# Performance work log

Measured on AMD Instinct MI355X. Metric: run time of the kernel, lower is better.

## Reference

```python
import jax, jax.numpy as jnp
import numpy as np

K = 20
EPS = 1e-5
NUM_CLASSES = 50


def knn_idx(x, k):
    # x: [B, C, N] -> [B, N, k] indices of k nearest neighbors (self included)
    xx = jnp.sum(x * x, axis=1)                      # [B, N]
    inner = jnp.einsum('bcn,bcm->bnm', x, x)         # [B, N, N]
    neg_dist = 2.0 * inner - xx[:, :, None] - xx[:, None, :]
    return jax.lax.top_k(neg_dist, k)[1]


def graph_feature(x, k):
    # x: [B, C, N] -> [B, 2C, N, k] edge features (feat - center, center)
    B = x.shape[0]
    idx = knn_idx(x, k)                              # [B, N, k]
    xt = jnp.transpose(x, (0, 2, 1))                 # [B, N, C]
    feat = xt[jnp.arange(B)[:, None, None], idx]     # [B, N, k, C]
    center = xt[:, :, None, :]
    out = jnp.concatenate([feat - center, jnp.broadcast_to(center, feat.shape)], axis=-1)
    return jnp.transpose(out, (0, 3, 1, 2))


def group_norm(x, groups, w, b):
    B, C = x.shape[0], x.shape[1]
    shp = x.shape
    xg = x.reshape(B, groups, -1)
    mu = jnp.mean(xg, axis=-1, keepdims=True)
    var = jnp.var(xg, axis=-1, keepdims=True)
    xn = ((xg - mu) * jax.lax.rsqrt(var + EPS)).reshape(shp)
    bshape = (1, C) + (1,) * (len(shp) - 2)
    return xn * w.reshape(bshape) + b.reshape(bshape)


def leaky(x):
    return jnp.where(x >= 0, x, 0.2 * x)


def edge_block(x, W, gw, gb, groups, k):
    f = graph_feature(x, k)                          # [B, 2C, N, k]
    h = jnp.einsum('oc,bcnk->bonk', W, f)            # 1x1 conv2d, no bias
    h = leaky(group_norm(h, groups, gw, gb))
    return jnp.max(h, axis=-1)                       # [B, Cout, N]


def conv1d(x, W, b):
    return jnp.einsum('oc,bcn->bon', W, x) + b[None, :, None]


def _mk(key, shape, fan_in):
    return jax.random.normal(key, shape, jnp.float32) * (1.0 / np.sqrt(fan_in))


def setup_inputs():
    key = jax.random.key(0)
    ks = jax.random.split(key, 32)
    B, N = 8, 2048
    d = {}
    d['x'] = jax.random.normal(ks[0], (B, 3, N), jnp.float32)
    d['W1'] = _mk(ks[1], (64, 6), 6)
    d['W2'] = _mk(ks[2], (64, 128), 128)
    d['W3'] = _mk(ks[3], (128, 128), 128)
    for i, (name, c) in enumerate([('g1', 64), ('g2', 64), ('g3', 128), ('gf', 1024), ('gs1', 512), ('gs2', 256), ('gs3', 128)]):
        d[name + 'w'] = 1.0 + 0.02 * jax.random.normal(ks[4 + 2 * i], (c,), jnp.float32)
        d[name + 'b'] = 0.02 * jax.random.normal(ks[5 + 2 * i], (c,), jnp.float32)
    d['Wm'] = _mk(ks[20], (1024, 256), 256)
    d['bm'] = jnp.zeros((1024,), jnp.float32)
    d['Ws1'] = _mk(ks[21], (512, 1280), 1280)
    d['bs1'] = jnp.zeros((512,), jnp.float32)
    d['Ws2'] = _mk(ks[22], (256, 512), 512)
    d['bs2'] = jnp.zeros((256,), jnp.float32)
    d['Ws3'] = _mk(ks[23], (128, 256), 256)
    d['bs3'] = jnp.zeros((128,), jnp.float32)
    d['Ws4'] = _mk(ks[24], (NUM_CLASSES, 128), 128)
    d['bs4'] = jnp.zeros((NUM_CLASSES,), jnp.float32)
    return d


def reference(x, W1, W2, W3, g1w, g1b, g2w, g2b, g3w, g3b, gfw, gfb, gs1w, gs1b, gs2w, gs2b, gs3w, gs3b, Wm, bm, Ws1, bs1, Ws2, bs2, Ws3, bs3, Ws4, bs4):
    B, _, N = x.shape
    x1 = edge_block(x, W1, g1w, g1b, 8, K)           # [B, 64, N]
    x2 = edge_block(x1, W2, g2w, g2b, 8, K)          # [B, 64, N]
    x3 = edge_block(x2, W3, g3w, g3b, 8, K)          # [B, 128, N]
    feats = jnp.concatenate([x1, x2, x3], axis=1)    # [B, 256, N]
    xb = jax.nn.relu(group_norm(conv1d(feats, Wm, bm), 32, gfw, gfb))  # [B, 1024, N]
    xmax = jnp.max(xb, axis=2)                       # [B, 1024]
    xmax_exp = jnp.broadcast_to(xmax[:, :, None], (B, 1024, N))
    combined = jnp.concatenate([xmax_exp, feats], axis=1)  # [B, 1280, N]
    h = jax.nn.relu(group_norm(conv1d(combined, Ws1, bs1), 16, gs1w, gs1b))
    h = jax.nn.relu(group_norm(conv1d(h, Ws2, bs2), 16, gs2w, gs2b))
    h = jax.nn.relu(group_norm(conv1d(h, Ws3, bs3), 8, gs3w, gs3b))
    logits = conv1d(h, Ws4, bs4)                     # [B, num_classes, N]
    return jax.nn.log_softmax(logits, axis=1)
```

## Files before the change

### kernel.cpp

```cpp
#include <hip/hip_runtime.h>

#define BN 8
#define NP 2048
#define KK 20
#define EPSV 1e-5f

typedef __attribute__((ext_vector_type(8))) short bf16x8;
typedef __attribute__((ext_vector_type(4))) float f32x4;

static __device__ __forceinline__ float leakyf(float v){ return v >= 0.f ? v : 0.2f*v; }
static __device__ __forceinline__ unsigned fenc(float f){
  unsigned u = __float_as_uint(f);
  unsigned m = (unsigned)((int)u >> 31);
  return u ^ (m | 0x80000000u);
}
static __device__ __forceinline__ float fdec(unsigned u){
  return __uint_as_float((u & 0x80000000u) ? (u & 0x7FFFFFFFu) : ~u);
}
static __device__ __forceinline__ unsigned bf2(float a, float b){
  unsigned ua = __float_as_uint(a), ub = __float_as_uint(b);
  ua = (ua + 0x7FFFu + ((ua>>16)&1u)) >> 16;
  ub = (ub + 0x7FFFu + ((ub>>16)&1u)) >> 16;
  return ua | (ub<<16);
}
static __device__ __forceinline__ unsigned short b16(float v){
  unsigned u = __float_as_uint(v);
  return (unsigned short)((u + 0x7FFFu + ((u>>16)&1u)) >> 16);
}
static __device__ __forceinline__ unsigned umax32(unsigned a, unsigned b){ return __builtin_elementwise_max(a,b); }
static __device__ __forceinline__ unsigned med3u(unsigned a, unsigned b, unsigned c){
  unsigned d;
  asm("v_med3_u32 %0, %1, %2, %3" : "=v"(d) : "v"(a), "v"(b), "v"(c));
  return d;
}

static __device__ __forceinline__ char* ldsW(char* base, int row, int colb){
  return base + row*80 + (colb ^ ((((unsigned)row>>3)&3u)<<4));
}
static __device__ __forceinline__ char* ldsX(char* base, int row, int colb){
  return base + row*80 + (colb ^ (((((unsigned)row>>2)^((unsigned)row>>4))&3u)<<4));
}
static __device__ __forceinline__ int swz128(int row, int colb){
  return (colb ^ ((row&7)<<4));
}

__global__ __launch_bounds__(256) void xx_kernel(const float* __restrict__ x, long ldb, int C,
                                                 float* __restrict__ xx){
  int b = blockIdx.y;
  int n = blockIdx.x*256 + threadIdx.x;
  const float* xp = x + (long)b*ldb + n;
  float a = 0.f;
  for(int c=0;c<C;c++){ float v = xp[(long)c*NP]; a += v*v; }
  xx[b*NP + n] = a;
}

static __device__ __forceinline__ void ins20(unsigned* tv, unsigned key){
  unsigned pold = tv[0];
  tv[0] = umax32(tv[0], key);
  #pragma unroll
  for(int r=1;r<20;r++){
    unsigned cold = tv[r];
    tv[r] = med3u(key, pold, cold);
    pold = cold;
  }
}

__global__ __launch_bounds__(256) void knnf_kernel(const unsigned short* __restrict__ fh,
                                                   const unsigned short* __restrict__ fl,
                                                   int cbase,
                                                   const float* __restrict__ xx,
                                                   unsigned* __restrict__ pk){
  __shared__ unsigned short CH[64][68];
  __shared__ unsigned short CL[64][68];
  __shared__ unsigned SK[64][68];
  __shared__ float cxs[64];
  const int b    = blockIdx.z;
  const int part = blockIdx.y;
  const int q0   = blockIdx.x*64;
  const int t    = threadIdx.x;
  const int lane = t & 63;
  const int w    = t >> 6;
  const int lr   = lane & 15, lg = lane >> 4;
  const unsigned short* fhb = fh + (long)b*NP*256;
  const unsigned short* flb = fl + (long)b*NP*128;
  const float* xxb = xx + b*NP;

  const unsigned short* qa = fhb + ((long)(q0 + w*16 + lr))*256 + cbase + lg*8;
  const unsigned short* qb = flb + ((long)(q0 + w*16 + lr))*128 + cbase + lg*8;
  bf16x8 ah0 = *(const bf16x8*)(qa);
  bf16x8 ah1 = *(const bf16x8*)(qa + 32);
  bf16x8 al0 = *(const bf16x8*)(qb);
  bf16x8 al1 = *(const bf16x8*)(qb + 32);
  float4 qxx4 = *(const float4*)(xxb + q0 + w*16 + lg*4);
  float qxx[4] = {qxx4.x, qxx4.y, qxx4.z, qxx4.w};

  unsigned tv[20];
  #pragma unroll
  for(int r=0;r<20;r++) tv[r] = 0u;
  const int sq = t>>2, sl = t&3;

  #define STAGE(ct_)                                                                        \
    {                                                                                       \
      const int ct__ = (ct_);                                                               \
      _Pragma("unroll")                                                                     \
      for(int i = t; i < 512; i += 256){                                                    \
        int row = i >> 3, seg = i & 7;                                                      \
        *(uint4*)&CH[row][seg*8] = *(const uint4*)(fhb + ((long)(ct__*64+row))*256 + cbase + seg*8); \
        *(uint4*)&CL[row][seg*8] = *(const uint4*)(flb + ((long)(ct__*64+row))*128 + cbase + seg*8); \
      }                                                                                     \
      if (t < 64) cxs[t] = xxb[ct__*64 + t];                                                \
    }

  STAGE(part*4);
  __syncthreads();

  #pragma unroll
  for(int cc=0; cc<4; cc++){
    __builtin_amdgcn_s_setprio(1);
    f32x4 acc[4];
    #pragma unroll
    for(int nt=0; nt<4; nt++){
      int crow = nt*16 + lr;
      bf16x8 bh0 = *(const bf16x8*)&CH[crow][lg*8];
      bf16x8 bh1 = *(const bf16x8*)&CH[crow][32 + lg*8];
      bf16x8 bl0 = *(const bf16x8*)&CL[crow][lg*8];
      bf16x8 bl1 = *(const bf16x8*)&CL[crow][32 + lg*8];
      f32x4 a = (f32x4){0.f,0.f,0.f,0.f};
      a = __builtin_amdgcn_mfma_f32_16x16x32_bf16(ah0, bh0, a, 0,0,0);
      a = __builtin_amdgcn_mfma_f32_16x16x32_bf16(ah1, bh1, a, 0,0,0);
      a = __builtin_amdgcn_mfma_f32_16x16x32_bf16(ah0, bl0, a, 0,0,0);
      a = __builtin_amdgcn_mfma_f32_16x16x32_bf16(ah1, bl1, a, 0,0,0);
      a = __builtin_amdgcn_mfma_f32_16x16x32_bf16(al0, bh0, a, 0,0,0);
      a = __builtin_amdgcn_mfma_f32_16x16x32_bf16(al1, bh1, a, 0,0,0);
      acc[nt] = a;
    }
    __builtin_amdgcn_s_setprio(0);
    float cxv[4];
    #pragma unroll
    for(int nt=0; nt<4; nt++) cxv[nt] = cxs[nt*16 + lr];
    unsigned key4[4][4];
    #pragma unroll
    for(int nt=0; nt<4; nt++){
      #pragma unroll
      for(int r=0;r<4;r++){
        float neg = 2.f*acc[nt][r] - qxx[r] - cxv[nt];
        key4[nt][r] = (fenc(neg) & 0xFFFFFF00u) | (255u - (unsigned)(cc*64 + nt*16 + lr));
      }
    }
    __syncthreads();
    #pragma unroll
    for(int nt=0; nt<4; nt++)
      #pragma unroll
      for(int r=0;r<4;r++)
        SK[w*16 + lg*4 + r][nt*16 + lr] = key4[nt][r];
    if (cc < 3){
      STAGE(part*4 + cc + 1);
    }
    __syncthreads();
    #pragma unroll
    for(int jj=0;jj<4;jj++){
      uint4 kv = *(const uint4*)&SK[sq][sl*16 + jj*4];
      ins20(tv, kv.x); ins20(tv, kv.y); ins20(tv, kv.z); ins20(tv, kv.w);
    }
  }
  #undef STAGE
  long base = ((((long)b*NP + q0 + sq)*8 + part)*4 + sl)*20;
  #pragma unroll
  for(int r=0;r<20;r++) pk[base+r] = tv[r];
}

__global__ __launch_bounds__(256) void knn1_kernel(const float* __restrict__ x,
                                                   const float* __restrict__ xx,
                                                   unsigned* __restrict__ pk){
  __shared__ float cx0[256], cx1[256], cx2[256], cxxa[256];
  const int b    = blockIdx.z;
  const int part = blockIdx.y;
  const int q0   = blockIdx.x*64;
  const int t    = threadIdx.x;
  const float* xb  = x + (long)b*3*NP;
  const float* xxb = xx + b*NP;

  cx0[t]  = xb[part*256 + t];
  cx1[t]  = xb[NP + part*256 + t];
  cx2[t]  = xb[2*NP + part*256 + t];
  cxxa[t] = xxb[part*256 + t];

  const int sq = t>>2, sl = t&3;
  const int q = q0 + sq;
  float qx = xb[q], qy = xb[NP + q], qz = xb[2*NP + q];
  float qxx = xxb[q];
  __syncthreads();

  unsigned tv[20];
  #pragma unroll
  for(int r=0;r<20;r++) tv[r] = 0u;

  for(int cc=0; cc<4; cc++){
    #pragma unroll
    for(int j=0;j<16;j++){
      int m = cc*64 + sl*16 + j;
      float ip = qx*cx0[m] + qy*cx1[m] + qz*cx2[m];
      float neg = 2.f*ip - qxx - cxxa[m];
      unsigned key = (fenc(neg) & 0xFFFFFF00u) | (255u - (unsigned)m);
      ins20(tv, key);
    }
  }
  long base = ((((long)b*NP + q0 + sq)*8 + part)*4 + sl)*20;
  #pragma unroll
  for(int r=0;r<20;r++) pk[base+r] = tv[r];
}

__global__ __launch_bounds__(256) void knnmerge_kernel(const unsigned* __restrict__ pk,
                                                       int* __restrict__ idxout){
  const int wid  = threadIdx.x >> 6;
  const int lane = threadIdx.x & 63;
  const long qg = (long)blockIdx.x*4 + wid;
  const unsigned* kb = pk + qg*640;
  const int l = lane >> 1, h = lane & 1;
  unsigned k[10];
  {
    const unsigned* src = kb + l*20 + h*10;
    #pragma unroll
    for(int i=0;i<10;i++) k[i] = src[i];
  }
  int rem = 10;
  int* op = idxout + qg*KK;
  const int gbase = (l>>2)*256;
  for(int r=0;r<KK;r++){
    unsigned key = k[0];
    int gi = gbase + 255 - (int)(key & 255u);
    unsigned long long cmp = (rem > 0)
        ? ((unsigned long long)(key & 0xFFFFFF00u) << 32) | (unsigned)(0x7FFFFFFF - gi)
        : 0ull;
    unsigned long long w = cmp;
    #pragma unroll
    for(int s=1;s<64;s<<=1){
      unsigned long long o = __shfl_xor(w, s, 64);
      w = (o > w) ? o : w;
    }
    if (lane == 0){
      op[r] = 0x7FFFFFFF - (int)(unsigned)(w & 0xFFFFFFFFu);
    }
    if (cmp == w){
      #pragma unroll
      for(int i=0;i<9;i++) k[i] = k[i+1];
      rem--;
    }
  }
}

template<int CIN, int O>
__global__ __launch_bounds__(256) void pcdual_kernel(const float* __restrict__ x, long ldb,
                                                     const float* __restrict__ W,
                                                     float* __restrict__ ya, float* __restrict__ dd){
  __shared__ float Wt[CIN][O+1];
  constexpr int NLOC = 256/O;
  const int b = blockIdx.y;
  const int n0 = blockIdx.x*NLOC;
  const int t = threadIdx.x;
  const int o = t % O;
  const int n = n0 + t/O;
  const float* xp = x + (long)b*ldb + n;
  float xv[CIN];
  #pragma unroll
  for(int c=0;c<CIN;c++) xv[c] = xp[(long)c*NP];
  for(int i=t;i<CIN*O;i+=256){ int oo=i/CIN, c=i%CIN; Wt[c][oo] = W[(long)oo*2*CIN + c]; }
  __syncthreads();
  float aa = 0.f;
  #pragma unroll
  for(int c=0;c<CIN;c++) aa += Wt[c][o]*xv[c];
  __syncthreads();
  for(int i=t;i<CIN*O;i+=256){ int oo=i/CIN, c=i%CIN; Wt[c][oo] = W[(long)oo*2*CIN + CIN + c]; }
  __syncthreads();
  float ab = 0.f;
  #pragma unroll
  for(int c=0;c<CIN;c++) ab += Wt[c][o]*xv[c];
  long outoff = ((long)b*NP + n)*O + o;
  ya[outoff] = aa;
  dd[outoff] = ab - aa;
}

template<int O>
__global__ __launch_bounds__(256) void pcdualm_kernel(const unsigned short* __restrict__ fh,
                                                      const unsigned short* __restrict__ fl,
                                                      int cbase,
                                                      const float* __restrict__ W,
                                                      float* __restrict__ ya, float* __restrict__ dd){
  __shared__ unsigned short AH[O][64];
  __shared__ unsigned short AL[O][64];
  __shared__ unsigned short DH[O][64];
  __shared__ unsigned short DL[O][64];
  const int b  = blockIdx.y;
  const int n0 = blockIdx.x*64;
  const int t  = threadIdx.x;
  const int lane = t & 63;
  const int w  = t >> 6;
  const int lr = lane & 15, lg = lane >> 4;

  for(int i=t; i<O*64; i+=256){
    int o = i >> 6, c = i & 63;
    float va = W[(long)o*128 + c];
    float vb = W[(long)o*128 + 64 + c];
    float vd = vb - va;
    unsigned short ah = b16(va);
    unsigned short dh = b16(vd);
    int byt = swz128(o, c*2);
    *(unsigned short*)((char*)&AH[o][0] + byt) = ah;
    *(unsigned short*)((char*)&AL[o][0] + byt) = b16(va - __uint_as_float(((unsigned)ah)<<16));
    *(unsigned short*)((char*)&DH[o][0] + byt) = dh;
    *(unsigned short*)((char*)&DL[o][0] + byt) = b16(vd - __uint_as_float(((unsigned)dh)<<16));
  }

  const int n = n0 + w*16 + lr;
  const unsigned short* xh = fh + ((long)b*NP + n)*256 + cbase + lg*8;
  const unsigned short* xl = fl + ((long)b*NP + n)*128 + cbase + lg*8;
  bf16x8 xh0 = *(const bf16x8*)(xh);
  bf16x8 xh1 = *(const bf16x8*)(xh + 32);
  bf16x8 xl0 = *(const bf16x8*)(xl);
  bf16x8 xl1 = *(const bf16x8*)(xl + 32);
  __syncthreads();

  #pragma unroll
  for(int mi=0; mi<O/16; mi++){
    int row = mi*16 + lr;
    bf16x8 a_h0 = *(const bf16x8*)((char*)&AH[row][0] + swz128(row, lg*16));
    bf16x8 a_h1 = *(const bf16x8*)((char*)&AH[row][0] + swz128(row, 64 + lg*16));
    bf16x8 a_l0 = *(const bf16x8*)((char*)&AL[row][0] + swz128(row, lg*16));
    bf16x8 a_l1 = *(const bf16x8*)((char*)&AL[row][0] + swz128(row, 64 + lg*16));
    f32x4 aa = (f32x4){0.f,0.f,0.f,0.f};
    aa = __builtin_amdgcn_mfma_f32_16x16x32_bf16(a_h0, xh0, aa, 0,0,0);
    aa = __builtin_amdgcn_mfma_f32_16x16x32_bf16(a_h1, xh1, aa, 0,0,0);
    aa = __builtin_amdgcn_mfma_f32_16x16x32_bf16(a_h0, xl0, aa, 0,0,0);
    aa = __builtin_amdgcn_mfma_f32_16x16x32_bf16(a_h1, xl1, aa, 0,0,0);
    aa = __builtin_amdgcn_mfma_f32_16x16x32_bf16(a_l0, xh0, aa, 0,0,0);
    aa = __builtin_amdgcn_mfma_f32_16x16x32_bf16(a_l1, xh1, aa, 0,0,0);
    bf16x8 d_h0 = *(const bf16x8*)((char*)&DH[row][0] + swz128(row, lg*16));
    bf16x8 d_h1 = *(const bf16x8*)((char*)&DH[row][0] + swz128(row, 64 + lg*16));
    bf16x8 d_l0 = *(const bf16x8*)((char*)&DL[row][0] + swz128(row, lg*16));
    bf16x8 d_l1 = *(const bf16x8*)((char*)&DL[row][0] + swz128(row, 64 + lg*16));
    f32x4 ad = (f32x4){0.f,0.f,0.f,0.f};
    ad = __builtin_amdgcn_mfma_f32_16x16x32_bf16(d_h0, xh0, ad, 0,0,0);
    ad = __builtin_amdgcn_mfma_f32_16x16x32_bf16(d_h1, xh1, ad, 0,0,0);
    ad = __builtin_amdgcn_mfma_f32_16x16x32_bf16(d_h0, xl0, ad, 0,0,0);
    ad = __builtin_amdgcn_mfma_f32_16x16x32_bf16(d_h1, xl1, ad, 0,0,0);
    ad = __builtin_amdgcn_mfma_f32_16x16x32_bf16(d_l0, xh0, ad, 0,0,0);
    ad = __builtin_amdgcn_mfma_f32_16x16x32_bf16(d_l1, xh1, ad, 0,0,0);
    long ooff = ((long)b*NP + n)*O + mi*16 + lg*4;
    float4 va = {aa[0],aa[1],aa[2],aa[3]};
    float4 vd = {ad[0],ad[1],ad[2],ad[3]};
    *(float4*)(ya + ooff) = va;
    *(float4*)(dd + ooff) = vd;
  }
}

template<int O>
__global__ __launch_bounds__(256) void egather_kernel(const float* __restrict__ ya, const float* __restrict__ dd,
                               const int* __restrict__ idx,
                               float* __restrict__ mx, float* __restrict__ mn,
                               float* __restrict__ stats){
  __shared__ float sred2[4][16];
  constexpr int NSUB = 256/O;
  constexpr int CPG = O/8;
  const int b  = blockIdx.x & 7;
  const int n0 = (blockIdx.x >> 3) * 32;
  const int t = threadIdx.x;
  const int w = t >> 6;
  const int o = t % O;
  const int ns = t / O;
  if (t < 64) sred2[t>>4][t&15] = 0.f;
  __syncthreads();
  float gs = 0.f, gs2 = 0.f;
  const float* yab = ya + (long)b*NP*O;
  for(int p=ns; p<32; p+=NSUB){
    int n = n0 + p;
    float d = dd[((long)b*NP + n)*O + o];
    const int* ip = idx + ((long)b*NP + n)*KK;
    float m = -__builtin_inff(), mm = __builtin_inff(), s = 0.f, s2 = 0.f;
    #pragma unroll
    for(int k=0;k<KK;k++){
      int j = ip[k];
      float v = yab[(long)j*O + o] + d;
      s += v; s2 += v*v;
      m = fmaxf(m, v); mm = fminf(mm, v);
    }
    mx[((long)b*NP + n)*O + o] = m;
    mn[((long)b*NP + n)*O + o] = mm;
    gs += s; gs2 += s2;
  }
  #pragma unroll
  for(int offm=1; offm<CPG; offm<<=1){
    gs  += __shfl_xor(gs,  offm, CPG);
    gs2 += __shfl_xor(gs2, offm, CPG);
  }
  if ((o & (CPG-1)) == 0){
    int g = o / CPG;
    sred2[w][g*2]   = gs;
    sred2[w][g*2+1] = gs2;
  }
  __syncthreads();
  if (t < 16){
    float a = sred2[0][t] + sred2[1][t] + sred2[2][t] + sred2[3][t];
    atomicAdd(&stats[b*16 + t], a);
  }
}

template<int O, bool NEEDXX, bool WRITEL>
__global__ __launch_bounds__(256) void enorm_kernel(const float* __restrict__ mx, const float* __restrict__ mn,
                                                    const float* __restrict__ stats,
                                                    const float* __restrict__ gw, const float* __restrict__ gb,
                                                    int coff,
                                                    float* __restrict__ xxout,
                                                    unsigned* __restrict__ fhout, unsigned* __restrict__ flout){
  __shared__ float lmx[64][65];
  __shared__ float lmn[64][65];
  const int b = blockIdx.z;
  const int o0 = blockIdx.y*64;
  const int n0 = blockIdx.x*64;
  const int t = threadIdx.x;
  for(int r=0;r<16;r++){
    int i = r*4 + t/64, j = t%64;
    long src = ((long)b*NP + n0 + i)*O + o0 + j;
    lmx[i][j] = mx[src];
    lmn[i][j] = mn[src];
  }
  __syncthreads();
  constexpr int CPG = O/8;
  const float inv_cnt = 1.f/((float)CPG*NP*KK);
  float xacc = 0.f;
  for(int r=0;r<16;r++){
    int ol = r*4 + t/64, nl = t%64;
    int og = o0 + ol;
    int g = og / CPG;
    float S  = stats[(b*8+g)*2];
    float S2 = stats[(b*8+g)*2+1];
    float mu = S*inv_cnt;
    float var = S2*inv_cnt - mu*mu;
    float rs = rsqrtf(var + EPSV);
    float w = gw[og], bb = gb[og];
    float sel = (w >= 0.f) ? lmx[nl][ol] : lmn[nl][ol];
    float v = leakyf((sel - mu)*rs*w + bb);
    lmx[nl][ol] = v;
    if (NEEDXX) xacc += v*v;
  }
  __syncthreads();
  {
    const int cb2 = (coff + o0) >> 1;
    #pragma unroll
    for(int k=0;k<8;k++){
      int flat = k*256 + t;
      int n = flat >> 5, cp = flat & 31;
      float v0 = lmx[n][2*cp], v1 = lmx[n][2*cp+1];
      unsigned short h0 = b16(v0), h1 = b16(v1);
      fhout[((long)b*NP + n0 + n)*128 + cb2 + cp] = (unsigned)h0 | ((unsigned)h1<<16);
      if (WRITEL){
        float r0 = v0 - __uint_as_float(((unsigned)h0)<<16);
        float r1 = v1 - __uint_as_float(((unsigned)h1)<<16);
        flout[((long)b*NP + n0 + n)*64 + cb2 + cp] =
            (unsigned)b16(r0) | ((unsigned)b16(r1)<<16);
      }
    }
  }
  if (NEEDXX){
    __syncthreads();
    float* red = &lmn[0][0];
    red[(t>>6)*64 + (t&63)] = xacc;
    __syncthreads();
    if (t < 64){
      float a = red[t] + red[64+t] + red[128+t] + red[192+t];
      xxout[b*NP + n0 + t] = a;
    }
  }
}

template<bool WRITE_Y, bool DO_STATS, bool DO_MAXMIN, bool IN_NORM, bool XBF16>
__global__ __launch_bounds__(256) void mgemm_kernel(
    const float* __restrict__ W, int ldw,
    const float* __restrict__ x, long xldb,
    const unsigned short* __restrict__ xbf,
    const float* __restrict__ bias, const float* __restrict__ basev,
    int O, int C, int gshift,
    float* __restrict__ y, float* __restrict__ stats,
    unsigned* __restrict__ mmax, unsigned* __restrict__ mmin,
    const float* __restrict__ instats, const float* __restrict__ igw,
    const float* __restrict__ igb, int igshift, float iinv)
{
  __shared__ __align__(16) char WlB[128*80];
  __shared__ __align__(16) char XtB[XBF16 ? 16 : 128*80];
  __shared__ float sred[16];
  __shared__ unsigned smax[128];
  __shared__ unsigned smin[128];

  const int b  = blockIdx.z;
  const int o0 = blockIdx.y*128;
  const int nb = blockIdx.x*128;
  const int t  = threadIdx.x;
  const int lane = t & 63;
  const int wid = t >> 6;
  const int wmo = wid >> 1, wno = wid & 1;
  const int lr = lane & 15, lg = lane >> 4;

  if (DO_STATS && t < 16) sred[t] = 0.f;
  if (DO_MAXMIN && t < 128){ smax[t] = 0u; smin[t] = 0xFFFFFFFFu; }

  f32x4 acc[4][4];
  #pragma unroll
  for(int i=0;i<4;i++)
    #pragma unroll
    for(int j=0;j<4;j++) acc[i][j] = (f32x4){0.f,0.f,0.f,0.f};

  const int so  = t & 127;
  const int scb = (t >> 7) << 5;
  const int xcg = t >> 5;
  const int xng = t & 31;

  for(int cc=0; cc<C; cc+=32){
    bf16x8 bfr[4];
    if (XBF16){
      #pragma unroll
      for(int nj=0;nj<4;nj++)
        bfr[nj] = *(const bf16x8*)(xbf + ((long)b*NP + nb + wno*64 + nj*16 + lr)*256 + cc + lg*8);
    }
    __syncthreads();
    {
      const float* wp = W + (long)(o0 + so)*ldw + cc + (scb>>1);
      #pragma unroll
      for(int j=0;j<4;j++){
        float4 f = *(const float4*)(wp + j*4);
        uint2 v = { bf2(f.x,f.y), bf2(f.z,f.w) };
        *(uint2*)ldsW(WlB, so, scb + j*8) = v;
      }
    }
    if (!XBF16){
      const float* xp = x + (long)b*xldb + (long)(cc + xcg*4)*NP + nb + xng*4;
      float4 f0 = *(const float4*)(xp);
      float4 f1 = *(const float4*)(xp + NP);
      float4 f2 = *(const float4*)(xp + 2*NP);
      float4 f3 = *(const float4*)(xp + 3*NP);
      float X4[4][4] = {{f0.x,f0.y,f0.z,f0.w},{f1.x,f1.y,f1.z,f1.w},
                        {f2.x,f2.y,f2.z,f2.w},{f3.x,f3.y,f3.z,f3.w}};
      if (IN_NORM){
        #pragma unroll
        for(int i=0;i<4;i++){
          int c = cc + xcg*4 + i;
          int g = c >> igshift;
          const float* sp = instats + ((long)b*(C>>igshift) + g)*2;
          float mu = sp[0]*iinv;
          float var = sp[1]*iinv - mu*mu;
          float rs = rsqrtf(var + EPSV);
          float aa = rs*igw[c];
          float c2 = igb[c] - mu*aa;
          #pragma unroll
          for(int j=0;j<4;j++) X4[i][j] = fmaxf(X4[i][j]*aa + c2, 0.f);
        }
      }
      #pragma unroll
      for(int j=0;j<4;j++){
        uint2 v = { bf2(X4[0][j], X4[1][j]), bf2(X4[2][j], X4[3][j]) };
        *(uint2*)ldsX(XtB, xng*4 + j, xcg*8) = v;
      }
    }
    __syncthreads();
    bf16x8 afr[4];
    #pragma unroll
    for(int mi=0;mi<4;mi++) afr[mi] = *(const bf16x8*)ldsW(WlB, wmo*64 + mi*16 + lr, lg*16);
    if (!XBF16){
      #pragma unroll
      for(int nj=0;nj<4;nj++) bfr[nj] = *(const bf16x8*)ldsX(XtB, wno*64 + nj*16 + lr, lg*16);
    }
    #pragma unroll
    for(int mi=0;mi<4;mi++)
      #pragma unroll
      for(int nj=0;nj<4;nj++)
        acc[mi][nj] = __builtin_amdgcn_mfma_f32_16x16x32_bf16(afr[mi], bfr[nj], acc[mi][nj], 0, 0, 0);
  }

  float bb4[4][4];
  #pragma unroll
  for(int mi=0;mi<4;mi++){
    #pragma unroll
    for(int r=0;r<4;r++){
      int o = o0 + wmo*64 + mi*16 + lg*4 + r;
      float v = 0.f;
      if (bias)  v += bias[o];
      if (basev) v += basev[(long)b*O + o];
      bb4[mi][r] = v;
    }
  }
  #pragma unroll
  for(int mi=0;mi<4;mi++)
    #pragma unroll
    for(int nj=0;nj<4;nj++)
      #pragma unroll
      for(int r=0;r<4;r++) acc[mi][nj][r] += bb4[mi][r];

  if (WRITE_Y){
    #pragma unroll
    for(int mi=0;mi<4;mi++)
      #pragma unroll
      for(int nj=0;nj<4;nj++)
        #pragma unroll
        for(int r=0;r<4;r++){
          int o = o0 + wmo*64 + mi*16 + lg*4 + r;
          y[((long)b*O + o)*NP + nb + wno*64 + nj*16 + lr] = acc[mi][nj][r];
        }
  }
  if (DO_STATS){
    #pragma unroll
    for(int mi=0;mi<4;mi++){
      float s = 0.f, s2 = 0.f;
      #pragma unroll
      for(int nj=0;nj<4;nj++)
        #pragma unroll
        for(int r=0;r<4;r++){ float v = acc[mi][nj][r]; s += v; s2 += v*v; }
      int gi = (wmo*64 + mi*16) >> gshift;
      atomicAdd(&sred[gi*2],   s);
      atomicAdd(&sred[gi*2+1], s2);
    }
  }
  if (DO_MAXMIN){
    #pragma unroll
    for(int mi=0;mi<4;mi++)
      #pragma unroll
      for(int r=0;r<4;r++){
        float mv = acc[mi][0][r], mw = acc[mi][0][r];
        #pragma unroll
        for(int nj=1;nj<4;nj++){ mv = fmaxf(mv, acc[mi][nj][r]); mw = fminf(mw, acc[mi][nj][r]); }
        int ol = wmo*64 + mi*16 + lg*4 + r;
        atomicMax(&smax[ol], fenc(mv));
        atomicMin(&smin[ol], fenc(mw));
      }
  }
  if (DO_STATS || DO_MAXMIN) __syncthreads();
  if (DO_STATS){
    int ngb = 128 >> gshift;
    if (t < ngb*2){
      atomicAdd(&stats[((long)b*(O>>gshift) + (o0>>gshift) + (t>>1))*2 + (t&1)], sred[t]);
    }
  }
  if (DO_MAXMIN){
    if (t < 128){
      atomicMax(&mmax[(long)b*O + o0 + t], smax[t]);
      atomicMin(&mmin[(long)b*O + o0 + t], smin[t]);
    }
  }
}

__global__ void xmax_kernel(const unsigned* __restrict__ mmax, const unsigned* __restrict__ mmin,
                            const float* __restrict__ stats, const float* __restrict__ gw,
                            const float* __restrict__ gb, float* __restrict__ xmax){
  int t = blockIdx.x*256 + threadIdx.x;
  int b = t >> 10, o = t & 1023;
  int g = o >> 5;
  const float* sp = stats + (b*32+g)*2;
  const float inv_cnt = 1.f/(32.f*NP);
  float mu = sp[0]*inv_cnt;
  float var = sp[1]*inv_cnt - mu*mu;
  float rs = rsqrtf(var + EPSV);
  float w = gw[o];
  float sel = (w >= 0.f) ? fdec(mmax[t]) : fdec(mmin[t]);
  float v = (sel - mu)*rs*w + gb[o];
  xmax[t] = fmaxf(v, 0.f);
}

__global__ __launch_bounds__(256) void base1_kernel(const float* __restrict__ Ws1, const float* __restrict__ bs1,
                                                    const float* __restrict__ xmax, float* __restrict__ base1){
  __shared__ float sred[4][8];
  const int o = blockIdx.x;
  const int t = threadIdx.x;
  const float* wp = Ws1 + (long)o*1280;
  float acc[8];
  #pragma unroll
  for(int bb=0;bb<8;bb++) acc[bb]=0.f;
  #pragma unroll
  for(int cc=0;cc<4;cc++){
    int c = cc*256 + t;
    float w = wp[c];
    #pragma unroll
    for(int bb=0;bb<8;bb++) acc[bb] += w * xmax[bb*1024 + c];
  }
  #pragma unroll
  for(int bb=0;bb<8;bb++){
    float a = acc[bb];
    a += __shfl_xor(a,1);  a += __shfl_xor(a,2);  a += __shfl_xor(a,4);
    a += __shfl_xor(a,8);  a += __shfl_xor(a,16); a += __shfl_xor(a,32);
    acc[bb]=a;
  }
  if ((t&63)==0){
    #pragma unroll
    for(int bb=0;bb<8;bb++) sred[t>>6][bb]=acc[bb];
  }
  __syncthreads();
  if (t<8){
    float a = sred[0][t]+sred[1][t]+sred[2][t]+sred[3][t] + bs1[o];
    base1[t*512 + o] = a;
  }
}

__global__ __launch_bounds__(256) void s4_kernel(const float* __restrict__ h3raw,
                                                 const float* __restrict__ stats,
                                                 const float* __restrict__ gw, const float* __restrict__ gb,
                                                 const float* __restrict__ W,
                                                 const float* __restrict__ bias,
                                                 float* __restrict__ out){
  const int b = blockIdx.y;
  const int n = blockIdx.x*64 + (threadIdx.x>>2);
  const int cl = threadIdx.x & 3;
  const float inv_cnt = 1.f/(16.f*NP);
  float mu0, rs0, mu1, rs1;
  {
    const float* sp = stats + (b*8 + cl*2)*2;
    mu0 = sp[0]*inv_cnt;
    float var = sp[1]*inv_cnt - mu0*mu0;
    rs0 = rsqrtf(var + EPSV);
    const float* sp1 = stats + (b*8 + cl*2 + 1)*2;
    mu1 = sp1[0]*inv_cnt;
    float var1 = sp1[1]*inv_cnt - mu1*mu1;
    rs1 = rsqrtf(var1 + EPSV);
  }
  float hv[32];
  #pragma unroll
  for(int c=0;c<32;c++){
    int og = cl*32 + c;
    float rs = (c < 16) ? rs0 : rs1;
    float mu = (c < 16) ? mu0 : mu1;
    float a = rs*gw[og];
    float c2 = gb[og] - mu*a;
    float v = h3raw[((long)b*128 + og)*NP + n];
    hv[c] = fmaxf(v*a + c2, 0.f);
  }
  float zz[50];
  #pragma unroll
  for(int o=0;o<50;o++){
    const float* wp = W + o*128 + cl*32;
    float a = 0.f;
    #pragma unroll
    for(int c=0;c<32;c++) a += wp[c]*hv[c];
    a += __shfl_xor(a,1);
    a += __shfl_xor(a,2);
    zz[o] = a + bias[o];
  }
  float m = zz[0];
  #pragma unroll
  for(int o=1;o<50;o++) m = fmaxf(m, zz[o]);
  float s = 0.f;
  #pragma unroll
  for(int o=0;o<50;o++) s += __expf(zz[o]-m);
  float lse = m + __logf(s);
  #pragma unroll
  for(int o=0;o<50;o++){
    if ((o&3)==cl) out[((long)b*50+o)*NP+n] = zz[o]-lse;
  }
}

extern "C" void kernel_launch(void* const* d_in, const int* in_sizes, int n_in,
                              void* d_out, int out_size, void* d_ws, size_t ws_size,
                              hipStream_t stream)
{
  const float* x   = (const float*)d_in[0];
  const float* W1  = (const float*)d_in[1];
  const float* W2  = (const float*)d_in[2];
  const float* W3  = (const float*)d_in[3];
  const float* g1w = (const float*)d_in[4];
  const float* g1b = (const float*)d_in[5];
  const float* g2w = (const float*)d_in[6];
  const float* g2b = (const float*)d_in[7];
  const float* g3w = (const float*)d_in[8];
  const float* g3b = (const float*)d_in[9];
  const float* gfw = (const float*)d_in[10];
  const float* gfb = (const float*)d_in[11];
  const float* gs1w= (const float*)d_in[12];
  const float* gs1b= (const float*)d_in[13];
  const float* gs2w= (const float*)d_in[14];
  const float* gs2b= (const float*)d_in[15];
  const float* gs3w= (const float*)d_in[16];
  const float* gs3b= (const float*)d_in[17];
  const float* Wm  = (const float*)d_in[18];
  const float* bm  = (const float*)d_in[19];
  const float* Ws1 = (const float*)d_in[20];
  const float* bs1 = (const float*)d_in[21];
  const float* Ws2 = (const float*)d_in[22];
  const float* bs2 = (const float*)d_in[23];
  const float* Ws3 = (const float*)d_in[24];
  const float* bs3 = (const float*)d_in[25];
  const float* Ws4 = (const float*)d_in[26];
  const float* bs4 = (const float*)d_in[27];
  float* out = (float*)d_out;

  char* ws = (char*)d_ws;
  size_t off = 0;
  auto alloc = [&](size_t bytes)->char*{
    char* p = ws + off;
    off += (bytes + 255) & ~(size_t)255;
    return p;
  };
  char* zbase = alloc(6656 + 32768);
  float* estats1 = (float*)(zbase + 0);
  float* estats2 = (float*)(zbase + 512);
  float* estats3 = (float*)(zbase + 1024);
  float* mstats  = (float*)(zbase + 1536);
  float* s1stats = (float*)(zbase + 3584);
  float* s2stats = (float*)(zbase + 4608);
  float* s3stats = (float*)(zbase + 5632);
  unsigned* mmax = (unsigned*)(zbase + 6656);
  unsigned* mmin = (unsigned*)alloc(32768);
  float* xmaxb = (float*)alloc(8*1024*4);
  float* base1 = (float*)alloc(8*512*4);
  int*   idxb  = (int*)  alloc((size_t)BN*NP*KK*4);
  float* xxb   = (float*)alloc((size_t)BN*NP*4);
  unsigned* fhb = (unsigned*)alloc((size_t)BN*NP*256*2);
  unsigned* flb = (unsigned*)alloc((size_t)BN*NP*128*2);
  float* ya    = (float*)alloc((size_t)BN*NP*128*4);
  float* dd    = (float*)alloc((size_t)BN*NP*128*4);
  float* mx    = (float*)alloc((size_t)BN*NP*128*4);
  float* mn    = (float*)alloc((size_t)BN*NP*128*4);
  float* ybuf1 = (float*)alloc((size_t)BN*512*NP*4);
  float* ybuf2 = (float*)alloc((size_t)BN*256*NP*4);
  float* ybuf3 = (float*)alloc((size_t)BN*128*NP*4);

  unsigned* pk = (unsigned*)ya;
  const unsigned short* fh16 = (const unsigned short*)fhb;
  const unsigned short* fl16 = (const unsigned short*)flb;

  hipMemsetAsync(zbase, 0, 6656 + 32768, stream);
  hipMemsetAsync(mmin, 0xFF, 32768, stream);

  dim3 blk256(256);

  xx_kernel<<<dim3(NP/256, BN), blk256, 0, stream>>>(x, (long)3*NP, 3, xxb);
  knn1_kernel<<<dim3(NP/64, 8, BN), blk256, 0, stream>>>(x, xxb, pk);
  knnmerge_kernel<<<dim3(BN*NP/4), blk256, 0, stream>>>(pk, idxb);
  pcdual_kernel<3,64><<<dim3(NP/4, BN), blk256, 0, stream>>>(x, (long)3*NP, W1, ya, dd);
  egather_kernel<64><<<dim3(8*NP/32), blk256, 0, stream>>>(ya, dd, idxb, mx, mn, estats1);
  enorm_kernel<64,true,true><<<dim3(NP/64, 1, BN), blk256, 0, stream>>>(
      mx, mn, estats1, g1w, g1b, 0, xxb, fhb, flb);

  knnf_kernel<<<dim3(NP/64, 8, BN), blk256, 0, stream>>>(fh16, fl16, 0, xxb, pk);
  knnmerge_kernel<<<dim3(BN*NP/4), blk256, 0, stream>>>(pk, idxb);
  pcdualm_kernel<64><<<dim3(NP/64, BN), blk256, 0, stream>>>(fh16, fl16, 0, W2, ya, dd);
  egather_kernel<64><<<dim3(8*NP/32), blk256, 0, stream>>>(ya, dd, idxb, mx, mn, estats2);
  enorm_kernel<64,true,true><<<dim3(NP/64, 1, BN), blk256, 0, stream>>>(
      mx, mn, estats2, g2w, g2b, 64, xxb, fhb, flb);

  knnf_kernel<<<dim3(NP/64, 8, BN), blk256, 0, stream>>>(fh16, fl16, 64, xxb, pk);
  knnmerge_kernel<<<dim3(BN*NP/4), blk256, 0, stream>>>(pk, idxb);
  pcdualm_kernel<128><<<dim3(NP/64, BN), blk256, 0, stream>>>(fh16, fl16, 64, W3, ya, dd);
  egather_kernel<128><<<dim3(8*NP/32), blk256, 0, stream>>>(ya, dd, idxb, mx, mn, estats3);
  enorm_kernel<128,false,false><<<dim3(NP/64, 2, BN), blk256, 0, stream>>>(
      mx, mn, estats3, g3w, g3b, 128, nullptr, fhb, nullptr);

  mgemm_kernel<false,true,true,false,true><<<dim3(16,8,BN), blk256, 0, stream>>>(
      Wm, 256, nullptr, 0, fh16, bm, nullptr, 1024, 256, 5,
      nullptr, mstats, mmax, mmin, nullptr, nullptr, nullptr, 0, 0.f);
  xmax_kernel<<<dim3(32), blk256, 0, stream>>>(mmax, mmin, mstats, gfw, gfb, xmaxb);
  base1_kernel<<<dim3(512), blk256, 0, stream>>>(Ws1, bs1, xmaxb, base1);

  mgemm_kernel<true,true,false,false,true><<<dim3(16,4,BN), blk256, 0, stream>>>(
      Ws1 + 1024, 1280, nullptr, 0, fh16, nullptr, base1, 512, 256, 5,
      ybuf1, s1stats, nullptr, nullptr, nullptr, nullptr, nullptr, 0, 0.f);

  mgemm_kernel<true,true,false,true,false><<<dim3(16,2,BN), blk256, 0, stream>>>(
      Ws2, 512, ybuf1, (long)512*NP, nullptr, bs2, nullptr, 256, 512, 4,
      ybuf2, s2stats, nullptr, nullptr, s1stats, gs1w, gs1b, 5, 1.f/(32.f*NP));

  mgemm_kernel<true,true,false,true,false><<<dim3(16,1,BN), blk256, 0, stream>>>(
      Ws3, 256, ybuf2, (long)256*NP, nullptr, bs3, nullptr, 128, 256, 4,
      ybuf3, s3stats, nullptr, nullptr, s2stats, gs2w, gs2b, 4, 1.f/(16.f*NP));

  s4_kernel<<<dim3(NP/64, BN), blk256, 0, stream>>>(ybuf3, s3stats, gs3w, gs3b, Ws4, bs4, out);
}
```

Baseline: 546.7 us.

## Pre-convert GEMM weights to bf16 and stage tiles through LDS in bf16 mgemm

Adds a weight-prep kernel that converts Wm and the feats slice of Ws1 to bf16 once per call. The bf16-input mgemm path then stages both weight and feature tiles into padded LDS with 16-byte loads, where before it converted fp32 weights per tile and read feature fragments straight from global memory. The next tile's staging comes after the compute barrier. This aims to cut per-tile conversion work and make global accesses coalesced, at the cost of two extra launches and more LDS per block.

```diff
diff --git a/kernel.cpp b/kernel.cpp
--- a/kernel.cpp
+++ b/kernel.cpp
@@ -42,6 +42,15 @@
 }
 static __device__ __forceinline__ int swz128(int row, int colb){
   return (colb ^ ((row&7)<<4));
+}
+
+__global__ __launch_bounds__(256) void wprep_kernel(const float* __restrict__ W, int ldw, int O,
+                                                    unsigned short* __restrict__ out){
+  long i = (long)blockIdx.x*256 + threadIdx.x;
+  if (i < (long)O*256){
+    int o = (int)(i >> 8), c = (int)(i & 255);
+    out[i] = b16(W[(long)o*ldw + c]);
+  }
 }
 
 __global__ __launch_bounds__(256) void xx_kernel(const float* __restrict__ x, long ldb, int C,
@@ -477,6 +486,7 @@
     const float* __restrict__ W, int ldw,
     const float* __restrict__ x, long xldb,
     const unsigned short* __restrict__ xbf,
+    const unsigned short* __restrict__ wbf,
     const float* __restrict__ bias, const float* __restrict__ basev,
     int O, int C, int gshift,
     float* __restrict__ y, float* __restrict__ stats,
@@ -484,8 +494,9 @@
     const float* __restrict__ instats, const float* __restrict__ igw,
     const float* __restrict__ igb, int igshift, float iinv)
 {
-  __shared__ __align__(16) char WlB[128*80];
-  __shared__ __align__(16) char XtB[XBF16 ? 16 : 128*80];
+  constexpr int SMB = XBF16 ? 128*136 : 128*80;
+  __shared__ __align__(16) char SA[SMB];
+  __shared__ __align__(16) char SB[SMB];
   __shared__ float sred[16];
   __shared__ unsigned smax[128];
   __shared__ unsigned smin[128];
@@ -508,70 +519,93 @@
     #pragma unroll
     for(int j=0;j<4;j++) acc[i][j] = (f32x4){0.f,0.f,0.f,0.f};
 
-  const int so  = t & 127;
-  const int scb = (t >> 7) << 5;
-  const int xcg = t >> 5;
-  const int xng = t & 31;
-
-  for(int cc=0; cc<C; cc+=32){
-    bf16x8 bfr[4];
-    if (XBF16){
-      #pragma unroll
-      for(int nj=0;nj<4;nj++)
-        bfr[nj] = *(const bf16x8*)(xbf + ((long)b*NP + nb + wno*64 + nj*16 + lr)*256 + cc + lg*8);
-    }
-    __syncthreads();
-    {
-      const float* wp = W + (long)(o0 + so)*ldw + cc + (scb>>1);
-      #pragma unroll
-      for(int j=0;j<4;j++){
-        float4 f = *(const float4*)(wp + j*4);
-        uint2 v = { bf2(f.x,f.y), bf2(f.z,f.w) };
-        *(uint2*)ldsW(WlB, so, scb + j*8) = v;
+  if (XBF16){
+    unsigned short (*WT)[68] = (unsigned short(*)[68])SA;
+    unsigned short (*XT)[68] = (unsigned short(*)[68])SB;
+    #define STAGEM(cc_)                                                                     \
+      {                                                                                     \
+        const int cc__ = (cc_);                                                             \
+        _Pragma("unroll")                                                                   \
+        for(int i = t; i < 512; i += 256){                                                  \
+          int row = i >> 2, seg = i & 3;                                                    \
+          *(uint4*)&WT[row][seg*8] = *(const uint4*)(wbf + (long)(o0+row)*256 + cc__ + seg*8); \
+          *(uint4*)&XT[row][seg*8] = *(const uint4*)(xbf + ((long)b*NP + nb + row)*256 + cc__ + seg*8); \
+        }                                                                                   \
       }
-    }
-    if (!XBF16){
-      const float* xp = x + (long)b*xldb + (long)(cc + xcg*4)*NP + nb + xng*4;
-      float4 f0 = *(const float4*)(xp);
-      float4 f1 = *(const float4*)(xp + NP);
-      float4 f2 = *(const float4*)(xp + 2*NP);
-      float4 f3 = *(const float4*)(xp + 3*NP);
-      float X4[4][4] = {{f0.x,f0.y,f0.z,f0.w},{f1.x,f1.y,f1.z,f1.w},
-                        {f2.x,f2.y,f2.z,f2.w},{f3.x,f3.y,f3.z,f3.w}};
-      if (IN_NORM){
+    STAGEM(0);
+    for(int cc=0; cc<C; cc+=32){
+      __syncthreads();
+      bf16x8 afr[4], bfr[4];
+      #pragma unroll
+      for(int mi=0;mi<4;mi++) afr[mi] = *(const bf16x8*)&WT[wmo*64 + mi*16 + lr][lg*8];
+      #pragma unroll
+      for(int nj=0;nj<4;nj++) bfr[nj] = *(const bf16x8*)&XT[wno*64 + nj*16 + lr][lg*8];
+      #pragma unroll
+      for(int mi=0;mi<4;mi++)
         #pragma unroll
-        for(int i=0;i<4;i++){
-          int c = cc + xcg*4 + i;
-          int g = c >> igshift;
-          const float* sp = instats + ((long)b*(C>>igshift) + g)*2;
-          float mu = sp[0]*iinv;
-          float var = sp[1]*iinv - mu*mu;
-          float rs = rsqrtf(var + EPSV);
-          float aa = rs*igw[c];
-          float c2 = igb[c] - mu*aa;
-          #pragma unroll
-          for(int j=0;j<4;j++) X4[i][j] = fmaxf(X4[i][j]*aa + c2, 0.f);
+        for(int nj=0;nj<4;nj++)
+          acc[mi][nj] = __builtin_amdgcn_mfma_f32_16x16x32_bf16(afr[mi], bfr[nj], acc[mi][nj], 0, 0, 0);
+      __syncthreads();
+      if (cc + 32 < C){ STAGEM(cc + 32); }
+    }
+    #undef STAGEM
+  } else {
+    const int so  = t & 127;
+    const int scb = (t >> 7) << 5;
+    const int xcg = t >> 5;
+    const int xng = t & 31;
+    for(int cc=0; cc<C; cc+=32){
+      __syncthreads();
+      {
+        const float* wp = W + (long)(o0 + so)*ldw + cc + (scb>>1);
+        #pragma unroll
+        for(int j=0;j<4;j++){
+          float4 f = *(const float4*)(wp + j*4);
+          uint2 v = { bf2(f.x,f.y), bf2(f.z,f.w) };
+          *(uint2*)ldsW(SA, so, scb + j*8) = v;
         }
       }
-      #pragma unroll
-      for(int j=0;j<4;j++){
-        uint2 v = { bf2(X4[0][j], X4[1][j]), bf2(X4[2][j], X4[3][j]) };
-        *(uint2*)ldsX(XtB, xng*4 + j, xcg*8) = v;
+      {
+        const float* xp = x + (long)b*xldb + (long)(cc + xcg*4)*NP + nb + xng*4;
+        float4 f0 = *(const float4*)(xp);
+        float4 f1 = *(const float4*)(xp + NP);
+        float4 f2 = *(const float4*)(xp + 2*NP);
+        float4 f3 = *(const float4*)(xp + 3*NP);
+        float X4[4][4] = {{f0.x,f0.y,f0.z,f0.w},{f1.x,f1.y,f1.z,f1.w},
+                          {f2.x,f2.y,f2.z,f2.w},{f3.x,f3.y,f3.z,f3.w}};
+        if (IN_NORM){
+          #pragma unroll
+          for(int i=0;i<4;i++){
+            int c = cc + xcg*4 + i;
+            int g = c >> igshift;
+            const float* sp = instats + ((long)b*(C>>igshift) + g)*2;
+            float mu = sp[0]*iinv;
+            float var = sp[1]*iinv - mu*mu;
+            float rs = rsqrtf(var + EPSV);
+            float aa = rs*igw[c];
+            float c2 = igb[c] - mu*aa;
+            #pragma unroll
+            for(int j=0;j<4;j++) X4[i][j] = fmaxf(X4[i][j]*aa + c2, 0.f);
+          }
+        }
+        #pragma unroll
+        for(int j=0;j<4;j++){
+          uint2 v = { bf2(X4[0][j], X4[1][j]), bf2(X4[2][j], X4[3][j]) };
+          *(uint2*)ldsX(SB, xng*4 + j, xcg*8) = v;
+        }
       }
-    }
-    __syncthreads();
-    bf16x8 afr[4];
-    #pragma unroll
-    for(int mi=0;mi<4;mi++) afr[mi] = *(const bf16x8*)ldsW(WlB, wmo*64 + mi*16 + lr, lg*16);
-    if (!XBF16){
-      #pragma unroll
-      for(int nj=0;nj<4;nj++) bfr[nj] = *(const bf16x8*)ldsX(XtB, wno*64 + nj*16 + lr, lg*16);
-    }
-    #pragma unroll
-    for(int mi=0;mi<4;mi++)
-      #pragma unroll
-      for(int nj=0;nj<4;nj++)
-        acc[mi][nj] = __builtin_amdgcn_mfma_f32_16x16x32_bf16(afr[mi], bfr[nj], acc[mi][nj], 0, 0, 0);
+      __syncthreads();
+      bf16x8 afr[4], bfr[4];
+      #pragma unroll
+      for(int mi=0;mi<4;mi++) afr[mi] = *(const bf16x8*)ldsW(SA, wmo*64 + mi*16 + lr, lg*16);
+      #pragma unroll
+      for(int nj=0;nj<4;nj++) bfr[nj] = *(const bf16x8*)ldsX(SB, wno*64 + nj*16 + lr, lg*16);
+      #pragma unroll
+      for(int mi=0;mi<4;mi++)
+        #pragma unroll
+        for(int nj=0;nj<4;nj++)
+          acc[mi][nj] = __builtin_amdgcn_mfma_f32_16x16x32_bf16(afr[mi], bfr[nj], acc[mi][nj], 0, 0, 0);
+    }
   }
 
   float bb4[4][4];
@@ -807,6 +841,8 @@
   float* base1 = (float*)alloc(8*512*4);
   int*   idxb  = (int*)  alloc((size_t)BN*NP*KK*4);
   float* xxb   = (float*)alloc((size_t)BN*NP*4);
+  unsigned short* wmb  = (unsigned short*)alloc((size_t)1024*256*2);
+  unsigned short* ws1b = (unsigned short*)alloc((size_t)512*256*2);
   unsigned* fhb = (unsigned*)alloc((size_t)BN*NP*256*2);
   unsigned* flb = (unsigned*)alloc((size_t)BN*NP*128*2);
   float* ya    = (float*)alloc((size_t)BN*NP*128*4);
@@ -826,6 +862,9 @@
 
   dim3 blk256(256);
 
+  wprep_kernel<<<dim3(1024), blk256, 0, stream>>>(Wm, 256, 1024, wmb);
+  wprep_kernel<<<dim3(512),  blk256, 0, stream>>>(Ws1 + 1024, 1280, 512, ws1b);
+
   xx_kernel<<<dim3(NP/256, BN), blk256, 0, stream>>>(x, (long)3*NP, 3, xxb);
   knn1_kernel<<<dim3(NP/64, 8, BN), blk256, 0, stream>>>(x, xxb, pk);
   knnmerge_kernel<<<dim3(BN*NP/4), blk256, 0, stream>>>(pk, idxb);
@@ -849,21 +888,21 @@
       mx, mn, estats3, g3w, g3b, 128, nullptr, fhb, nullptr);
 
   mgemm_kernel<false,true,true,false,true><<<dim3(16,8,BN), blk256, 0, stream>>>(
-      Wm, 256, nullptr, 0, fh16, bm, nullptr, 1024, 256, 5,
+      nullptr, 0, nullptr, 0, fh16, wmb, bm, nullptr, 1024, 256, 5,
       nullptr, mstats, mmax, mmin, nullptr, nullptr, nullptr, 0, 0.f);
   xmax_kernel<<<dim3(32), blk256, 0, stream>>>(mmax, mmin, mstats, gfw, gfb, xmaxb);
   base1_kernel<<<dim3(512), blk256, 0, stream>>>(Ws1, bs1, xmaxb, base1);
 
   mgemm_kernel<true,true,false,false,true><<<dim3(16,4,BN), blk256, 0, stream>>>(
-      Ws1 + 1024, 1280, nullptr, 0, fh16, nullptr, base1, 512, 256, 5,
+      nullptr, 0, nullptr, 0, fh16, ws1b, nullptr, base1, 512, 256, 5,
       ybuf1, s1stats, nullptr, nullptr, nullptr, nullptr, nullptr, 0, 0.f);
 
   mgemm_kernel<true,true,false,true,false><<<dim3(16,2,BN), blk256, 0, stream>>>(
-      Ws2, 512, ybuf1, (long)512*NP, nullptr, bs2, nullptr, 256, 512, 4,
+      Ws2, 512, ybuf1, (long)512*NP, nullptr, nullptr, bs2, nullptr, 256, 512, 4,
       ybuf2, s2stats, nullptr, nullptr, s1stats, gs1w, gs1b, 5, 1.f/(32.f*NP));
 
   mgemm_kernel<true,true,false,true,false><<<dim3(16,1,BN), blk256, 0, stream>>>(
-      Ws3, 256, ybuf2, (long)256*NP, nullptr, bs3, nullptr, 128, 256, 4,
+      Ws3, 256, ybuf2, (long)256*NP, nullptr, nullptr, bs3, nullptr, 128, 256, 4,
       ybuf3, s3stats, nullptr, nullptr, s2stats, gs2w, gs2b, 4, 1.f/(16.f*NP));
 
   s4_kernel<<<dim3(NP/64, BN), blk256, 0, stream>>>(ybuf3, s3stats, gs3w, gs3b, Ws4, bs4, out);
```

After: 570.8 us. 4.4% more time.
